# Kernel tuning notes

Measured on AMD Instinct MI355X. Metric: run time of the kernel, lower is better.

## Reference

```python
import jax, jax.numpy as jnp
import numpy as np

D = 1024

def setup_inputs() -> dict:
    key = jax.random.key(0)
    k1, k2, k3, k4 = jax.random.split(key, 4)
    context = jax.random.normal(k1, (32, 2048, D), dtype=jnp.float32)
    # nn.Linear(dim, dim, bias=False): weight [D, D], applied as x @ W.T
    W = jax.random.normal(k2, (D, D), dtype=jnp.float32) / np.sqrt(D)
    # nn.Linear(dim, 1): weight [1, D], bias [1]
    v = jax.random.normal(k3, (D,), dtype=jnp.float32) / np.sqrt(D)
    b = jax.random.normal(k4, (), dtype=jnp.float32) * 0.01
    return {"context": context, "W": W, "v": v, "b": b}

def reference(context, W, v, b):
    # context: [B, S, D]
    h = jnp.tanh(jnp.einsum('bsd,ed->bse', context, W))      # [B, S, D]
    attn_logits = jnp.einsum('bsd,d->bs', h, v) + b          # [B, S]
    attn = jax.nn.softmax(attn_logits, axis=-1)              # softmax over sourceL
    weighted_context = jnp.einsum('bs,bsd->bd', attn, context)
    return weighted_context, attn
```

## Files before the change

kernel.cpp:

```cpp
#include <hip/hip_runtime.h>
#include <stdint.h>

#define BDIM 32
#define SDIM 2048
#define DDIM 1024
#define MDIM (BDIM * SDIM)

typedef __bf16 bf16x8 __attribute__((ext_vector_type(8)));
typedef float  f32x4  __attribute__((ext_vector_type(4)));


__device__ inline unsigned short f2bf(float f) {
  union { float f; unsigned u; } un; un.f = f;
  unsigned r = un.u + 0x7fffu + ((un.u >> 16) & 1u);
  return (unsigned short)(r >> 16);
}

__device__ inline float fast_tanh(float x) {
  float e = __expf(2.0f * x);
  return 1.0f - 2.0f / (e + 1.0f);
}

__device__ inline void gl_lds16(const unsigned short* g, unsigned short* l) {
  __builtin_amdgcn_global_load_lds(
      (__attribute__((address_space(1))) unsigned int*)(void*)(uintptr_t)g,
      (__attribute__((address_space(3))) unsigned int*)l,
      16, 0, 0);
}


__global__ __launch_bounds__(256) void cvt_kernel(const float* __restrict__ src,
                                                  unsigned short* __restrict__ dst) {
  size_t i = (size_t)blockIdx.x * 256 + threadIdx.x;
  const float4* s4 = (const float4*)src;
  float4 a = s4[2 * i];
  float4 b = s4[2 * i + 1];
  uint4 o;
  o.x = (unsigned)f2bf(a.x) | ((unsigned)f2bf(a.y) << 16);
  o.y = (unsigned)f2bf(a.z) | ((unsigned)f2bf(a.w) << 16);
  o.z = (unsigned)f2bf(b.x) | ((unsigned)f2bf(b.y) << 16);
  o.w = (unsigned)f2bf(b.z) | ((unsigned)f2bf(b.w) << 16);
  ((uint4*)dst)[i] = o;
}


__global__ __launch_bounds__(256) void gemm_logits(
    const unsigned short* __restrict__ A,
    const unsigned short* __restrict__ Bw,
    const float* __restrict__ v,
    float* __restrict__ logits)
{
  __shared__ __align__(16) unsigned short Al[128 * 32];
  __shared__ __align__(16) unsigned short Bl[128 * 32];

  const int t  = threadIdx.x;
  const int mt = blockIdx.x >> 3;
  const int nt = blockIdx.x & 7;
  const int m0 = mt * 128;
  const int n0 = nt * 128;
  const int w    = t >> 6;
  const int lane = t & 63;
  const int wm = (w >> 1) * 64;
  const int wn = (w & 1) * 64;
  const int c = lane & 15;
  const int q = lane >> 4;

  float vv[4];
#pragma unroll
  for (int ni = 0; ni < 4; ++ni) vv[ni] = v[n0 + wn + ni * 16 + c];

  f32x4 acc[4][4] = {};

  const int srow = t >> 2;
  const int skel = (t & 3) * 8;
  const unsigned short* ga0 = A  + (size_t)(m0 + srow) * DDIM + skel;
  const unsigned short* ga1 = A  + (size_t)(m0 + 64 + srow) * DDIM + skel;
  const unsigned short* gb0 = Bw + (size_t)(n0 + srow) * DDIM + skel;
  const unsigned short* gb1 = Bw + (size_t)(n0 + 64 + srow) * DDIM + skel;
  unsigned short* la0 = Al + w * 512;
  unsigned short* la1 = Al + 2048 + w * 512;
  unsigned short* lb0 = Bl + w * 512;
  unsigned short* lb1 = Bl + 2048 + w * 512;

  for (int kt = 0; kt < 32; ++kt) {
    const int k0 = kt * 32;
    gl_lds16(ga0 + k0, la0);
    gl_lds16(ga1 + k0, la1);
    gl_lds16(gb0 + k0, lb0);
    gl_lds16(gb1 + k0, lb1);
    __syncthreads();

    bf16x8 af[4], bfr[4];
#pragma unroll
    for (int mi = 0; mi < 4; ++mi)
      af[mi] = *(const bf16x8*)&Al[(wm + mi * 16 + c) * 32 + q * 8];
#pragma unroll
    for (int ni = 0; ni < 4; ++ni)
      bfr[ni] = *(const bf16x8*)&Bl[(wn + ni * 16 + c) * 32 + q * 8];

#pragma unroll
    for (int mi = 0; mi < 4; ++mi)
#pragma unroll
      for (int ni = 0; ni < 4; ++ni)
        acc[mi][ni] = __builtin_amdgcn_mfma_f32_16x16x32_bf16(
            af[mi], bfr[ni], acc[mi][ni], 0, 0, 0);

    __syncthreads();
  }

#pragma unroll
  for (int mi = 0; mi < 4; ++mi) {
    float p0 = 0.f, p1 = 0.f, p2 = 0.f, p3 = 0.f;
#pragma unroll
    for (int ni = 0; ni < 4; ++ni) {
      const float vvn = vv[ni];
      p0 += fast_tanh(acc[mi][ni][0]) * vvn;
      p1 += fast_tanh(acc[mi][ni][1]) * vvn;
      p2 += fast_tanh(acc[mi][ni][2]) * vvn;
      p3 += fast_tanh(acc[mi][ni][3]) * vvn;
    }
#pragma unroll
    for (int mask = 1; mask <= 8; mask <<= 1) {
      p0 += __shfl_xor(p0, mask);
      p1 += __shfl_xor(p1, mask);
      p2 += __shfl_xor(p2, mask);
      p3 += __shfl_xor(p3, mask);
    }
    if (c == 0) {
      float* lp = logits + (m0 + wm + mi * 16 + q * 4);
      atomicAdd(lp + 0, p0);
      atomicAdd(lp + 1, p1);
      atomicAdd(lp + 2, p2);
      atomicAdd(lp + 3, p3);
    }
  }
}


__global__ __launch_bounds__(256) void softmax_kernel(float* __restrict__ la) {
  const int b = blockIdx.x;
  const int t = threadIdx.x;
  float* p = la + (size_t)b * SDIM;
  float x[8];
#pragma unroll
  for (int i = 0; i < 8; ++i) x[i] = p[i * 256 + t];
  float m = x[0];
#pragma unroll
  for (int i = 1; i < 8; ++i) m = fmaxf(m, x[i]);
#pragma unroll
  for (int mask = 1; mask < 64; mask <<= 1) m = fmaxf(m, __shfl_xor(m, mask));
  __shared__ float redm[4], reds[4];
  const int w = t >> 6, lane = t & 63;
  if (lane == 0) redm[w] = m;
  __syncthreads();
  m = fmaxf(fmaxf(redm[0], redm[1]), fmaxf(redm[2], redm[3]));
  float e[8];
  float s = 0.f;
#pragma unroll
  for (int i = 0; i < 8; ++i) { e[i] = __expf(x[i] - m); s += e[i]; }
#pragma unroll
  for (int mask = 1; mask < 64; mask <<= 1) s += __shfl_xor(s, mask);
  if (lane == 0) reds[w] = s;
  __syncthreads();
  s = reds[0] + reds[1] + reds[2] + reds[3];
  const float inv = 1.0f / s;
#pragma unroll
  for (int i = 0; i < 8; ++i) p[i * 256 + t] = e[i] * inv;
}


__global__ __launch_bounds__(256) void wsum_kernel(const float* __restrict__ ctx,
                                                   const float* __restrict__ attn,
                                                   float* __restrict__ wc) {
  const int b  = blockIdx.x >> 4;
  const int sc = blockIdx.x & 15;
  const int t  = threadIdx.x;
  const float* cp = ctx + ((size_t)b * SDIM + sc * 128) * DDIM + t * 4;
  const float* ap = attn + (size_t)b * SDIM + sc * 128;
  float4 acc = {0.f, 0.f, 0.f, 0.f};
  for (int s = 0; s < 128; ++s) {
    const float a = ap[s];
    const float4 cv = *(const float4*)(cp + (size_t)s * DDIM);
    acc.x += a * cv.x; acc.y += a * cv.y; acc.z += a * cv.z; acc.w += a * cv.w;
  }
  float* o = wc + (size_t)b * DDIM + t * 4;
  atomicAdd(o + 0, acc.x);
  atomicAdd(o + 1, acc.y);
  atomicAdd(o + 2, acc.z);
  atomicAdd(o + 3, acc.w);
}


extern "C" void kernel_launch(void* const* d_in, const int* in_sizes, int n_in,
                              void* d_out, int out_size, void* d_ws, size_t ws_size,
                              hipStream_t stream) {
  const float* ctx = (const float*)d_in[0];
  const float* W   = (const float*)d_in[1];
  const float* v   = (const float*)d_in[2];

  float* out_wc   = (float*)d_out;
  float* out_attn = out_wc + BDIM * DDIM;

  unsigned short* ctx_bf = (unsigned short*)d_ws;
  unsigned short* W_bf   = ctx_bf + (size_t)MDIM * DDIM;

  hipMemsetAsync(d_out, 0, (size_t)out_size * sizeof(float), stream);

  cvt_kernel<<<(MDIM * DDIM) / (256 * 8), 256, 0, stream>>>(ctx, ctx_bf);
  cvt_kernel<<<(DDIM * DDIM) / (256 * 8), 256, 0, stream>>>(W, W_bf);
  gemm_logits<<<(MDIM / 128) * (DDIM / 128), 256, 0, stream>>>(ctx_bf, W_bf, v, out_attn);
  softmax_kernel<<<BDIM, 256, 0, stream>>>(out_attn);
  wsum_kernel<<<BDIM * 16, 256, 0, stream>>>(ctx, out_attn, out_wc);
}
```

Measured before the change: 618.0 us.

## Double GEMM K-tile with XOR-swizzled LDS and widen weighted-sum parallelism

The logits GEMM now stages 64-wide K tiles instead of 32, halving the number of barrier pairs per block. It also XOR-swizzles the LDS layout by row so that fragment reads avoid bank conflicts. The weighted-sum kernel splits the sequence into 64-row chunks across twice as many blocks, keeps attention weights in shared memory, and uses four independent accumulators so more loads are in flight. The cost is double the LDS per GEMM block, which may reduce occupancy, plus more atomic adds on the output.

After: 634.9 us. +2.7%, slower.

```diff
diff --git a/kernel.cpp b/kernel.cpp
--- a/kernel.cpp
+++ b/kernel.cpp
@@ -50,8 +50,8 @@
     const float* __restrict__ v,
     float* __restrict__ logits)
 {
-  __shared__ __align__(16) unsigned short Al[128 * 32];
-  __shared__ __align__(16) unsigned short Bl[128 * 32];
+  __shared__ __align__(16) unsigned short Al[128 * 64];
+  __shared__ __align__(16) unsigned short Bl[128 * 64];
 
   const int t  = threadIdx.x;
   const int mt = blockIdx.x >> 3;
@@ -71,39 +71,55 @@
 
   f32x4 acc[4][4] = {};
 
-  const int srow = t >> 2;
-  const int skel = (t & 3) * 8;
-  const unsigned short* ga0 = A  + (size_t)(m0 + srow) * DDIM + skel;
-  const unsigned short* ga1 = A  + (size_t)(m0 + 64 + srow) * DDIM + skel;
-  const unsigned short* gb0 = Bw + (size_t)(n0 + srow) * DDIM + skel;
-  const unsigned short* gb1 = Bw + (size_t)(n0 + 64 + srow) * DDIM + skel;
-  unsigned short* la0 = Al + w * 512;
-  unsigned short* la1 = Al + 2048 + w * 512;
-  unsigned short* lb0 = Bl + w * 512;
-  unsigned short* lb1 = Bl + 2048 + w * 512;
-
-  for (int kt = 0; kt < 32; ++kt) {
-    const int k0 = kt * 32;
-    gl_lds16(ga0 + k0, la0);
-    gl_lds16(ga1 + k0, la1);
-    gl_lds16(gb0 + k0, lb0);
-    gl_lds16(gb1 + k0, lb1);
+  const int srow = t >> 3;
+  const int scc  = ((t & 7) ^ (srow & 7)) * 8;
+  const unsigned short* gA[4];
+  const unsigned short* gB[4];
+  unsigned short* lA[4];
+  unsigned short* lB[4];
+#pragma unroll
+  for (int p = 0; p < 4; ++p) {
+    gA[p] = A  + (size_t)(m0 + p * 32 + srow) * DDIM + scc;
+    gB[p] = Bw + (size_t)(n0 + p * 32 + srow) * DDIM + scc;
+    lA[p] = Al + p * 2048 + w * 512;
+    lB[p] = Bl + p * 2048 + w * 512;
+  }
+
+  const int xr = c & 7;
+  int arow[4], brow[4], koff[2];
+#pragma unroll
+  for (int mi = 0; mi < 4; ++mi) arow[mi] = (wm + mi * 16 + c) * 64;
+#pragma unroll
+  for (int ni = 0; ni < 4; ++ni) brow[ni] = (wn + ni * 16 + c) * 64;
+#pragma unroll
+  for (int ks = 0; ks < 2; ++ks) koff[ks] = ((ks * 4 + q) ^ xr) * 8;
+
+  for (int kt = 0; kt < 16; ++kt) {
+    const int k0 = kt * 64;
+#pragma unroll
+    for (int p = 0; p < 4; ++p) {
+      gl_lds16(gA[p] + k0, lA[p]);
+      gl_lds16(gB[p] + k0, lB[p]);
+    }
     __syncthreads();
 
-    bf16x8 af[4], bfr[4];
-#pragma unroll
-    for (int mi = 0; mi < 4; ++mi)
-      af[mi] = *(const bf16x8*)&Al[(wm + mi * 16 + c) * 32 + q * 8];
-#pragma unroll
-    for (int ni = 0; ni < 4; ++ni)
-      bfr[ni] = *(const bf16x8*)&Bl[(wn + ni * 16 + c) * 32 + q * 8];
-
-#pragma unroll
-    for (int mi = 0; mi < 4; ++mi)
+#pragma unroll
+    for (int ks = 0; ks < 2; ++ks) {
+      bf16x8 af[4], bfr[4];
+#pragma unroll
+      for (int mi = 0; mi < 4; ++mi)
+        af[mi] = *(const bf16x8*)&Al[arow[mi] + koff[ks]];
 #pragma unroll
       for (int ni = 0; ni < 4; ++ni)
-        acc[mi][ni] = __builtin_amdgcn_mfma_f32_16x16x32_bf16(
-            af[mi], bfr[ni], acc[mi][ni], 0, 0, 0);
+        bfr[ni] = *(const bf16x8*)&Bl[brow[ni] + koff[ks]];
+
+#pragma unroll
+      for (int mi = 0; mi < 4; ++mi)
+#pragma unroll
+        for (int ni = 0; ni < 4; ++ni)
+          acc[mi][ni] = __builtin_amdgcn_mfma_f32_16x16x32_bf16(
+              af[mi], bfr[ni], acc[mi][ni], 0, 0, 0);
+    }
 
     __syncthreads();
   }
@@ -172,22 +188,35 @@
 __global__ __launch_bounds__(256) void wsum_kernel(const float* __restrict__ ctx,
                                                    const float* __restrict__ attn,
                                                    float* __restrict__ wc) {
-  const int b  = blockIdx.x >> 4;
-  const int sc = blockIdx.x & 15;
+  const int b  = blockIdx.x >> 5;
+  const int sc = blockIdx.x & 31;
   const int t  = threadIdx.x;
-  const float* cp = ctx + ((size_t)b * SDIM + sc * 128) * DDIM + t * 4;
-  const float* ap = attn + (size_t)b * SDIM + sc * 128;
-  float4 acc = {0.f, 0.f, 0.f, 0.f};
-  for (int s = 0; s < 128; ++s) {
-    const float a = ap[s];
-    const float4 cv = *(const float4*)(cp + (size_t)s * DDIM);
-    acc.x += a * cv.x; acc.y += a * cv.y; acc.z += a * cv.z; acc.w += a * cv.w;
-  }
+  __shared__ float as_[64];
+  if (t < 64) as_[t] = attn[(size_t)b * SDIM + sc * 64 + t];
+  __syncthreads();
+  const float* cp = ctx + ((size_t)b * SDIM + sc * 64) * DDIM + t * 4;
+  float4 a0 = {0.f, 0.f, 0.f, 0.f}, a1 = a0, a2 = a0, a3 = a0;
+#pragma unroll 4
+  for (int s = 0; s < 64; s += 4) {
+    const float4 c0 = *(const float4*)(cp + (size_t)(s + 0) * DDIM);
+    const float4 c1 = *(const float4*)(cp + (size_t)(s + 1) * DDIM);
+    const float4 c2 = *(const float4*)(cp + (size_t)(s + 2) * DDIM);
+    const float4 c3 = *(const float4*)(cp + (size_t)(s + 3) * DDIM);
+    const float w0 = as_[s], w1 = as_[s + 1], w2 = as_[s + 2], w3 = as_[s + 3];
+    a0.x += w0 * c0.x; a0.y += w0 * c0.y; a0.z += w0 * c0.z; a0.w += w0 * c0.w;
+    a1.x += w1 * c1.x; a1.y += w1 * c1.y; a1.z += w1 * c1.z; a1.w += w1 * c1.w;
+    a2.x += w2 * c2.x; a2.y += w2 * c2.y; a2.z += w2 * c2.z; a2.w += w2 * c2.w;
+    a3.x += w3 * c3.x; a3.y += w3 * c3.y; a3.z += w3 * c3.z; a3.w += w3 * c3.w;
+  }
+  a0.x += a1.x + a2.x + a3.x;
+  a0.y += a1.y + a2.y + a3.y;
+  a0.z += a1.z + a2.z + a3.z;
+  a0.w += a1.w + a2.w + a3.w;
   float* o = wc + (size_t)b * DDIM + t * 4;
-  atomicAdd(o + 0, acc.x);
-  atomicAdd(o + 1, acc.y);
-  atomicAdd(o + 2, acc.z);
-  atomicAdd(o + 3, acc.w);
+  atomicAdd(o + 0, a0.x);
+  atomicAdd(o + 1, a0.y);
+  atomicAdd(o + 2, a0.z);
+  atomicAdd(o + 3, a0.w);
 }
 
 
@@ -210,5 +239,5 @@
   cvt_kernel<<<(DDIM * DDIM) / (256 * 8), 256, 0, stream>>>(W, W_bf);
   gemm_logits<<<(MDIM / 128) * (DDIM / 128), 256, 0, stream>>>(ctx_bf, W_bf, v, out_attn);
   softmax_kernel<<<BDIM, 256, 0, stream>>>(out_attn);
-  wsum_kernel<<<BDIM * 16, 256, 0, stream>>>(ctx, out_attn, out_wc);
-}
+  wsum_kernel<<<BDIM * 32, 256, 0, stream>>>(ctx, out_attn, out_wc);
+}
```
